# Kernel optimization log

Hardware: AMD Instinct MI355X
Metric: run time of the kernel (lower is better)

## Reference

```python
import jax, jax.numpy as jnp
import numpy as np

B, S, H = 2, 2048, 2048
NH, NKV, HD = 32, 8, 64
GROUPS = NH // NKV
SCALE = HD ** -0.5


def _rope_tables(key):
    # Real RoPE cos/sin tables (HF Llama style), shape [B, S, HD]
    inv_freq = 1.0 / (10000.0 ** (jnp.arange(0, HD, 2, dtype=jnp.float32) / HD))  # [HD/2]
    t = jnp.arange(S, dtype=jnp.float32)
    freqs = jnp.outer(t, inv_freq)                      # [S, HD/2]
    emb = jnp.concatenate([freqs, freqs], axis=-1)      # [S, HD]
    cos = jnp.broadcast_to(jnp.cos(emb)[None], (B, S, HD))
    sin = jnp.broadcast_to(jnp.sin(emb)[None], (B, S, HD))
    return cos, sin


def setup_inputs() -> dict:
    key = jax.random.key(0)
    ks = jax.random.split(key, 9)
    w = 0.02
    cos, sin = _rope_tables(key)
    return {
        "hidden_states": jax.random.normal(ks[0], (B, S, H), jnp.float32),
        "bounding_box_embeddings": jax.random.normal(ks[1], (B, S, H), jnp.float32),
        "cos": cos,
        "sin": sin,
        "Wq": jax.random.normal(ks[2], (H, NH * HD), jnp.float32) * w,
        "Wk": jax.random.normal(ks[3], (H, NKV * HD), jnp.float32) * w,
        "Wv": jax.random.normal(ks[4], (H, NKV * HD), jnp.float32) * w,
        "Wo": jax.random.normal(ks[5], (NH * HD, H), jnp.float32) * w,
        "Wsq": jax.random.normal(ks[6], (H, NH * HD), jnp.float32) * w,
        "Wsk": jax.random.normal(ks[7], (H, NKV * HD), jnp.float32) * w,
    }


def _rotate_half(x):
    x1, x2 = x[..., : HD // 2], x[..., HD // 2 :]
    return jnp.concatenate([-x2, x1], axis=-1)


def _apply_rope(q, k, cos, sin):
    # q: [B,NH,S,HD], k: [B,NKV,S,HD]; cos/sin [B,S,HD] -> broadcast over heads
    c = cos[:, None, :, :]
    s = sin[:, None, :, :]
    return q * c + _rotate_half(q) * s, k * c + _rotate_half(k) * s


def _proj_heads(x, W, n_heads):
    b, s, _ = x.shape
    return (x @ W).reshape(b, s, n_heads, HD).transpose(0, 2, 1, 3)  # [B,nh,S,HD]


def reference(hidden_states, bounding_box_embeddings, cos, sin, Wq, Wk, Wv, Wo, Wsq, Wsk):
    # Text Q/K/V with RoPE
    q = _proj_heads(hidden_states, Wq, NH)
    k = _proj_heads(hidden_states, Wk, NKV)
    v = _proj_heads(hidden_states, Wv, NKV)
    q, k = _apply_rope(q, k, cos, sin)
    # Spatial Q/K (no V) with RoPE
    sq = _proj_heads(bounding_box_embeddings, Wsq, NH)
    sk = _proj_heads(bounding_box_embeddings, Wsk, NKV)
    sq, sk = _apply_rope(sq, sk, cos, sin)
    # Fused text+spatial states, then GQA repeat_kv
    q = q + sq                                   # [B,NH,S,HD]
    k = jnp.repeat(k + sk, GROUPS, axis=1)       # [B,NH,S,HD]
    v = jnp.repeat(v, GROUPS, axis=1)            # [B,NH,S,HD]
    # Eager attention with causal mask
    scores = jnp.einsum("bhqd,bhkd->bhqk", q, k) * SCALE
    causal = jnp.tril(jnp.ones((S, S), dtype=bool))
    scores = jnp.where(causal[None, None], scores, jnp.finfo(jnp.float32).min)
    probs = jax.nn.softmax(scores.astype(jnp.float32), axis=-1).astype(q.dtype)
    attn = jnp.einsum("bhqk,bhkd->bhqd", probs, v)           # [B,NH,S,HD]
    attn = attn.transpose(0, 2, 1, 3).reshape(B, S, NH * HD)  # [B,S,NH*HD]
    return attn @ Wo
```

## Files before the change

### kernel.cpp

```cpp
#include <hip/hip_runtime.h>

#define B_ 2
#define S_ 2048
#define H_ 2048
#define NH_ 32
#define NKV_ 8
#define HD_ 64

typedef short short8 __attribute__((ext_vector_type(8)));
typedef float f32x4 __attribute__((ext_vector_type(4)));
typedef float f32x16 __attribute__((ext_vector_type(16)));
typedef unsigned int uint4v __attribute__((ext_vector_type(4)));

__device__ __forceinline__ float bf2f(unsigned short u) {
  union { unsigned int i; float f; } v; v.i = ((unsigned int)u) << 16; return v.f;
}
__device__ __forceinline__ unsigned short f2bf(float f) {
  union { float f; unsigned int i; } v; v.f = f;
  unsigned int u = v.i;
  u += 0x7fffu + ((u >> 16) & 1u);
  return (unsigned short)(u >> 16);
}
__device__ __forceinline__ unsigned int cvtpk(float lo, float hi) {
  unsigned int r;
  asm("v_cvt_pk_bf16_f32 %0, %1, %2" : "=v"(r) : "v"(lo), "v"(hi));
  return r;
}
__device__ __forceinline__ void pl32swap(unsigned int& a, unsigned int& b) {
  asm("v_permlane32_swap_b32 %0, %1" : "+v"(a), "+v"(b));
}
__device__ __forceinline__ short8 mkfrag(unsigned a, unsigned b, unsigned c, unsigned d) {
  union { uint4v u; short8 s; } x;
  x.u = (uint4v){a, b, c, d};
  return x.s;
}
__device__ __forceinline__ void gload_lds16(const unsigned short* g, unsigned short* l) {
  __builtin_amdgcn_global_load_lds((const __attribute__((address_space(1))) void*)g,
                                   (__attribute__((address_space(3))) void*)l,
                                   16, 0, 0);
}
#define MFMA32(A, B, C) __builtin_amdgcn_mfma_f32_32x32x16_bf16(A, B, C, 0, 0, 0)
#define BARF() asm volatile("s_barrier" ::: "memory")

__global__ __launch_bounds__(256) void castA_frag(const float* __restrict__ in,
                                                  unsigned short* __restrict__ out) {
  int c = blockIdx.x * 4 + (threadIdx.x >> 6);
  int l = threadIdx.x & 63;
  int D = c & 31, KT = (c >> 5) & 31, bm = c >> 10;
  int row = bm * 256 + ((D >> 4) & 1) * 128 + ((D >> 3) & 1) * 64 + ((D >> 1) & 3) * 16 + (l & 15);
  int k = KT * 64 + (D & 1) * 32 + (l >> 4) * 8;
  const float* src = in + (size_t)row * 2048 + k;
  float4 v0 = *(const float4*)src;
  float4 v1 = *(const float4*)(src + 4);
  ushort4 o0, o1;
  o0.x = f2bf(v0.x); o0.y = f2bf(v0.y); o0.z = f2bf(v0.z); o0.w = f2bf(v0.w);
  o1.x = f2bf(v1.x); o1.y = f2bf(v1.y); o1.z = f2bf(v1.z); o1.w = f2bf(v1.w);
  unsigned short* dst = out + (size_t)c * 512 + l * 8;
  *(ushort4*)dst = o0;
  *(ushort4*)(dst + 4) = o1;
}

__global__ __launch_bounds__(256) void castW_frag(const float* __restrict__ W0,
                                                  const float* __restrict__ W1,
                                                  const float* __restrict__ W2,
                                                  unsigned short* __restrict__ out) {
  __shared__ float tile[64][33];
  int c = blockIdx.x;
  int ngroup = c & 7, KT = (c >> 3) & 31, bn = c >> 8;
  int n0 = bn * 256 + ngroup * 32;
  const float* W; int Nw, nb;
  if (n0 < 2048)      { W = W0; Nw = 2048; nb = n0; }
  else if (n0 < 2560) { W = W1; Nw = 512;  nb = n0 - 2048; }
  else                { W = W2; Nw = 512;  nb = n0 - 2560; }
  int t = threadIdx.x;
  int col = t & 31, r8 = t >> 5;
#pragma unroll
  for (int p = 0; p < 8; ++p) {
    int kk = p * 8 + r8;
    tile[kk][col] = W[(size_t)(KT * 64 + kk) * Nw + nb + col];
  }
  __syncthreads();
  int e = t >> 6, l = t & 63;
  int nf = e >> 1, ks = e & 1;
  ushort4 o0, o1;
  unsigned short* op = (unsigned short*)&o0;
#pragma unroll
  for (int j = 0; j < 8; ++j) {
    unsigned short v = f2bf(tile[ks * 32 + (l >> 4) * 8 + j][nf * 16 + (l & 15)]);
    if (j < 4) op[j] = v; else ((unsigned short*)&o1)[j - 4] = v;
  }
  unsigned short* dst = out + (((size_t)(c >> 3) * 32 + ngroup * 4 + e) << 9) + l * 8;
  *(ushort4*)dst = o0;
  *(ushort4*)(dst + 4) = o1;
}

__global__ __launch_bounds__(256) void transpose_cast(const float* __restrict__ W,
                                                      unsigned short* __restrict__ Wt,
                                                      int N, int K) {
  __shared__ float tile[32][33];
  int n0 = blockIdx.x * 32, k0 = blockIdx.y * 32;
  int tx = threadIdx.x & 31;
  int ty = threadIdx.x >> 5;
#pragma unroll
  for (int i = 0; i < 32; i += 8)
    tile[ty + i][tx] = W[(size_t)(k0 + ty + i) * N + n0 + tx];
  __syncthreads();
#pragma unroll
  for (int i = 0; i < 32; i += 8)
    Wt[(size_t)(n0 + ty + i) * K + k0 + tx] = f2bf(tile[tx][ty + i]);
}

__global__ __launch_bounds__(256) void vtrans_kernel(const unsigned short* __restrict__ P1,
                                                     unsigned short* __restrict__ Vt) {
  __shared__ unsigned short tile[32][33];
  int s0 = blockIdx.x * 32, d0 = blockIdx.y * 32, bk = blockIdx.z;
  int b = bk >> 3, kv = bk & 7;
  int tx = threadIdx.x & 31, ty = threadIdx.x >> 5;
#pragma unroll
  for (int i = 0; i < 32; i += 8)
    tile[ty + i][tx] = P1[(size_t)(b * S_ + s0 + ty + i) * 3072 + 2560 + kv * 64 + d0 + tx];
  __syncthreads();
#pragma unroll
  for (int i = 0; i < 32; i += 8)
    Vt[(size_t)(bk * 64 + d0 + ty + i) * S_ + s0 + tx] = tile[tx][ty + i];
}

__global__ __launch_bounds__(256) void combine_rope(const unsigned short* __restrict__ P1,
                                                    const unsigned short* __restrict__ P2,
                                                    const float* __restrict__ cosT,
                                                    const float* __restrict__ sinT,
                                                    unsigned short* __restrict__ Qb,
                                                    unsigned short* __restrict__ Kb) {
  int id = blockIdx.x * 256 + threadIdx.x;
  int row = id / 640;
  int grp = id - row * 640;
  int b = row >> 11;
  int s = row & 2047;
  bool isQ = grp < 512;
  int n = isQ ? grp * 4 : (grp - 512) * 4;
  int h = n >> 6;
  int d = n & 63;
  int base = isQ ? 0 : 2048;
  const int ld1 = 3072, ld2 = 2560;
  int pd = (d < 32) ? d + 32 : d - 32;
  float sign = (d < 32) ? -1.f : 1.f;
  int pcol = base + h * 64 + pd;

  ushort4 a1 = *(const ushort4*)&P1[(size_t)row * ld1 + base + n];
  ushort4 a2 = *(const ushort4*)&P2[(size_t)row * ld2 + base + n];
  ushort4 b1 = *(const ushort4*)&P1[(size_t)row * ld1 + pcol];
  ushort4 b2 = *(const ushort4*)&P2[(size_t)row * ld2 + pcol];
  float4 cv = *(const float4*)&cosT[(size_t)row * 64 + d];
  float4 sv = *(const float4*)&sinT[(size_t)row * 64 + d];
  float scale = isQ ? 0.125f : 1.0f;

  float xs[4] = { bf2f(a1.x) + bf2f(a2.x), bf2f(a1.y) + bf2f(a2.y),
                  bf2f(a1.z) + bf2f(a2.z), bf2f(a1.w) + bf2f(a2.w) };
  float xp[4] = { bf2f(b1.x) + bf2f(b2.x), bf2f(b1.y) + bf2f(b2.y),
                  bf2f(b1.z) + bf2f(b2.z), bf2f(b1.w) + bf2f(b2.w) };
  float cc[4] = { cv.x, cv.y, cv.z, cv.w };
  float ss[4] = { sv.x, sv.y, sv.z, sv.w };
  ushort4 o;
  unsigned short* op = (unsigned short*)&o;
#pragma unroll
  for (int i = 0; i < 4; ++i)
    op[i] = f2bf((xs[i] * cc[i] + sign * xp[i] * ss[i]) * scale);

  if (isQ)
    *(ushort4*)&Qb[((size_t)(b * NH_ + h) * S_ + s) * HD_ + d] = o;
  else
    *(ushort4*)&Kb[((size_t)(b * NKV_ + h) * S_ + s) * HD_ + d] = o;
}


#define RD_A(BC, MH) do { \
  _Pragma("unroll") for (int mf = 0; mf < 4; ++mf) { \
    _Pragma("unroll") for (int ks = 0; ks < 2; ++ks) \
      a[mf][ks] = *(const short8*)&lds[BC][((wm * 2 + (MH)) * 8 + mf * 2 + ks) * 512 + l * 8]; \
  } \
} while (0)

#define RD_B(BC, NH, DST) do { \
  _Pragma("unroll") for (int nf = 0; nf < 2; ++nf) { \
    _Pragma("unroll") for (int ks = 0; ks < 2; ++ks) \
      DST[nf][ks] = *(const short8*)&lds[BC][16384 + (((wn * 2 + (NH)) * 2 + nf) * 2 + ks) * 512 + l * 8]; \
  } \
} while (0)

#define MM(MH, NH, BB) do { \
  _Pragma("unroll") for (int mf = 0; mf < 4; ++mf) { \
    _Pragma("unroll") for (int nf = 0; nf < 2; ++nf) { \
      _Pragma("unroll") for (int ks = 0; ks < 2; ++ks) \
        acc[(MH) * 4 + mf][(NH) * 2 + nf] = __builtin_amdgcn_mfma_f32_16x16x32_bf16( \
            a[mf][ks], BB[nf][ks], acc[(MH) * 4 + mf][(NH) * 2 + nf], 0, 0, 0); \
    } \
  } \
} while (0)

#define STAGE_A(H, KT) do { \
  int bq_ = (KT) & 1; \
  int d1_ = (H) * 8 + w; \
  gload_lds16(aF + (((size_t)((KT) * 32 + d1_)) << 9), &lds[bq_][d1_ * 512]); \
  gload_lds16(aF + (((size_t)((KT) * 32 + 16 + d1_)) << 9), &lds[bq_][(16 + d1_) * 512]); \
} while (0)

#define STAGE_B(H, KT) do { \
  int bq_ = (KT) & 1; \
  int e1_ = (w >> 2) * 8 + (H) * 4 + (w & 3); \
  gload_lds16(bF + (((size_t)((KT) * 32 + e1_)) << 9), &lds[bq_][16384 + e1_ * 512]); \
  gload_lds16(bF + (((size_t)((KT) * 32 + 16 + e1_)) << 9), &lds[bq_][16384 + (16 + e1_) * 512]); \
} while (0)

#define GROUP_P(BC, G) do { \
  int kt1 = (G) + 1; if (kt1 > 31) kt1 = 31; \
  int kt2 = (G) + 2; if (kt2 > 31) kt2 = 31; \
  int BN_ = kt1 & 1; \
   \
  BARF(); \
  __builtin_amdgcn_s_setprio(1); MM(0, 0, b0); __builtin_amdgcn_s_setprio(0); \
  RD_B(BC, 1, b1); \
  STAGE_A(1, kt1); \
   \
  BARF(); \
  __builtin_amdgcn_s_setprio(1); MM(0, 1, b1); __builtin_amdgcn_s_setprio(0); \
  STAGE_A(0, kt2); \
   \
  BARF(); \
  RD_A(BC, 1); \
  __builtin_amdgcn_s_setprio(1); MM(1, 0, b0); __builtin_amdgcn_s_setprio(0); \
  STAGE_B(0, kt2); \
  asm volatile("s_waitcnt vmcnt(8)" ::: "memory"); \
   \
  BARF(); \
  __builtin_amdgcn_s_setprio(1); MM(1, 1, b1); __builtin_amdgcn_s_setprio(0); \
  RD_A(BN_, 0); \
  RD_B(BN_, 0, b0); \
  STAGE_B(1, kt2); \
  asm volatile("s_waitcnt vmcnt(6)" ::: "memory"); \
} while (0)

template <int OF32>
__global__ __launch_bounds__(512, 2) void gemm256(const unsigned short* __restrict__ Afr,
                                                  const unsigned short* __restrict__ Wfr,
                                                  void* __restrict__ Cv,
                                                  int N, int nbx) {
  __shared__ unsigned short lds[2][32768];
  int nwg = gridDim.x;
  int orig = blockIdx.x;
  int wgid = (orig & 7) * (nwg >> 3) + (orig >> 3);
  int bn = wgid % nbx, bm = wgid / nbx;
  int t = threadIdx.x, w = t >> 6, l = t & 63;
  int wm = w >> 2, wn = w & 3;

  const unsigned short* aF = Afr + ((size_t)bm << 19) + l * 8;
  const unsigned short* bF = Wfr + ((size_t)bn << 19) + l * 8;

  short8 a[4][2], b0[2][2], b1[2][2];
  f32x4 acc[8][4];
#pragma unroll
  for (int mi = 0; mi < 8; ++mi)
#pragma unroll
    for (int ni = 0; ni < 4; ++ni) acc[mi][ni] = 0.f;

  STAGE_A(0, 0); STAGE_A(1, 0); STAGE_B(0, 0); STAGE_B(1, 0);
  STAGE_A(0, 1); STAGE_B(0, 1); STAGE_B(1, 1);
  asm volatile("s_waitcnt vmcnt(6)" ::: "memory");
  BARF();
  RD_A(0, 0);
  RD_B(0, 0, b0);

  for (int tg = 0; tg < 32; tg += 2) {
    GROUP_P(0, tg);
    GROUP_P(1, tg + 1);
  }
  asm volatile("s_waitcnt vmcnt(0)" ::: "memory");

#pragma unroll
  for (int mi = 0; mi < 8; ++mi) {
    int row = bm * 256 + wm * 128 + (mi >> 2) * 64 + (mi & 3) * 16 + (l >> 4) * 4;
#pragma unroll
    for (int ni = 0; ni < 4; ++ni) {
      int col = bn * 256 + wn * 64 + (ni >> 1) * 32 + (ni & 1) * 16 + (l & 15);
#pragma unroll
      for (int r = 0; r < 4; ++r) {
        if constexpr (OF32)
          ((float*)Cv)[(size_t)(row + r) * N + col] = acc[mi][ni][r];
        else
          ((unsigned short*)Cv)[(size_t)(row + r) * N + col] = f2bf(acc[mi][ni][r]);
      }
    }
  }
}

#define RD_BN(BC) do { \
  _Pragma("unroll") for (int nf = 0; nf < 2; ++nf) { \
    _Pragma("unroll") for (int ks = 0; ks < 2; ++ks) \
      bb[nf][ks] = *(const short8*)&lds2[BC][16384 + ((wn * 2 + nf) * 2 + ks) * 512 + l * 8]; \
  } \
} while (0)

#define RD_AN(BC, MH) do { \
  _Pragma("unroll") for (int mf = 0; mf < 4; ++mf) { \
    _Pragma("unroll") for (int ks = 0; ks < 2; ++ks) \
      a[mf][ks] = *(const short8*)&lds2[BC][((wm * 2 + (MH)) * 8 + mf * 2 + ks) * 512 + l * 8]; \
  } \
} while (0)

#define MMN(MH) do { \
  _Pragma("unroll") for (int mf = 0; mf < 4; ++mf) { \
    _Pragma("unroll") for (int nf = 0; nf < 2; ++nf) { \
      _Pragma("unroll") for (int ks = 0; ks < 2; ++ks) \
        acc[(MH) * 4 + mf][nf] = __builtin_amdgcn_mfma_f32_16x16x32_bf16( \
            a[mf][ks], bb[nf][ks], acc[(MH) * 4 + mf][nf], 0, 0, 0); \
    } \
  } \
} while (0)

#define STAGE_AU(Q, KT) do { \
  int bq_ = (KT) & 1; \
  gload_lds16((((Q) < 2) ? srcA0 : srcA1) + (size_t)((Q) & 1) * (64 * 2048) + (size_t)(KT) * 64, \
              &lds2[bq_][(((Q) >> 1) * 16 + ((Q) & 1) * 8 + w) * 512]); \
} while (0)

#define STAGE_BU(H, KT) do { \
  int bq_ = (KT) & 1; \
  gload_lds16(srcB0 + (size_t)(H) * (32 * 2048) + (size_t)(KT) * 64, \
              &lds2[bq_][16384 + ((w >> 2) * 8 + (H) * 4 + (w & 3)) * 512]); \
} while (0)

#define GROUPN(BC, G) do { \
  int kt1 = (G) + 1; if (kt1 > 31) kt1 = 31; \
  int kt2 = (G) + 2; if (kt2 > 31) kt2 = 31; \
  RD_AN(BC, 0); RD_BN(BC); \
  STAGE_AU(1, kt1); STAGE_AU(3, kt1); \
  BARF(); \
  __builtin_amdgcn_s_setprio(1); MMN(0); __builtin_amdgcn_s_setprio(0); \
  BARF(); \
  RD_AN(BC, 1); \
  STAGE_AU(0, kt2); STAGE_AU(2, kt2); STAGE_BU(0, kt2); STAGE_BU(1, kt2); \
  BARF(); \
  __builtin_amdgcn_s_setprio(1); MMN(1); __builtin_amdgcn_s_setprio(0); \
  asm volatile("s_waitcnt vmcnt(4)" ::: "memory"); \
  BARF(); \
} while (0)

__global__ __launch_bounds__(512, 2) void gemm256n(const unsigned short* __restrict__ A,
                                                   const unsigned short* __restrict__ Bt,
                                                   float* __restrict__ C,
                                                   int N, int nbx) {
  __shared__ unsigned short lds2[2][24576];
  int nwg = gridDim.x;
  int orig = blockIdx.x;
  int wgid = (orig & 7) * (nwg >> 3) + (orig >> 3);
  int bn = wgid % nbx, bm = wgid / nbx;
  int t = threadIdx.x, w = t >> 6, l = t & 63;
  int wm = w >> 2, wn = w & 3;

  int kcol = (w & 1) * 32 + ((t >> 4) & 3) * 8;
  int rA0 = bm * 256 + ((w >> 1) & 3) * 16 + (t & 15);
  const unsigned short* srcA0 = A + (size_t)rA0 * 2048 + kcol;
  const unsigned short* srcA1 = srcA0 + (size_t)128 * 2048;
  int nB0 = bn * 128 + (w >> 2) * 64 + ((w >> 1) & 1) * 16 + (t & 15);
  const unsigned short* srcB0 = Bt + (size_t)nB0 * 2048 + kcol;

  short8 a[4][2], bb[2][2];
  f32x4 acc[8][2];
#pragma unroll
  for (int mi = 0; mi < 8; ++mi)
#pragma unroll
    for (int ni = 0; ni < 2; ++ni) acc[mi][ni] = 0.f;

  STAGE_AU(0, 0); STAGE_AU(1, 0); STAGE_AU(2, 0); STAGE_AU(3, 0); STAGE_BU(0, 0); STAGE_BU(1, 0);
  STAGE_AU(0, 1); STAGE_AU(2, 1); STAGE_BU(0, 1); STAGE_BU(1, 1);
  asm volatile("s_waitcnt vmcnt(4)" ::: "memory");
  BARF();

  for (int tg = 0; tg < 32; tg += 2) {
    GROUPN(0, tg);
    GROUPN(1, tg + 1);
  }
  asm volatile("s_waitcnt vmcnt(0)" ::: "memory");

#pragma unroll
  for (int mi = 0; mi < 8; ++mi) {
    int row = bm * 256 + wm * 128 + (mi >> 2) * 64 + (mi & 3) * 16 + (l >> 4) * 4;
#pragma unroll
    for (int nf = 0; nf < 2; ++nf) {
      int col = bn * 128 + wn * 32 + nf * 16 + (l & 15);
#pragma unroll
      for (int r = 0; r < 4; ++r)
        C[(size_t)(row + r) * N + col] = acc[mi][nf][r];
    }
  }
}

__global__ __launch_bounds__(512) void attn_kernel(const unsigned short* __restrict__ Q,
                                                   const unsigned short* __restrict__ K,
                                                   const unsigned short* __restrict__ Vt,
                                                   unsigned short* __restrict__ attnOut) {
  __shared__ unsigned short lK[2][64 * 64];
  __shared__ unsigned short lV[2][64 * 64];

  int bx = blockIdx.x;
  int j = bx & 7;
  int bh = bx >> 3;
  int head = bh & 31;
  int b = bh >> 5;
  int kvh = head >> 2;
  const unsigned short* Kp = K + (size_t)(b * NKV_ + kvh) * S_ * HD_;
  const unsigned short* Vp = Vt + (size_t)(b * NKV_ + kvh) * HD_ * S_;

  int t = threadIdx.x;
  int w = t >> 6, l = t & 63;
  int q32 = l & 31, hf = l >> 5;
  int qb_eff = (w < 4) ? j : (15 - j);
  int qbase_w = qb_eff * 128 + (w & 3) * 32;
  const unsigned short* Qp = Q + ((size_t)(b * NH_ + head) * S_ + qbase_w) * HD_;

  short8 qf[4];
  {
    const unsigned short* qrow = Qp + (size_t)q32 * HD_ + hf * 8;
#pragma unroll
    for (int kc = 0; kc < 4; ++kc)
      qf[kc] = *(const short8*)(qrow + kc * 16);
  }

  int srow = t >> 3;
  int sslot = t & 7;
  unsigned lOff = srow * 128 + ((sslot ^ (srow & 7)) << 4);
  const char* gK0 = (const char*)(Kp + (size_t)srow * 64 + sslot * 8);
  const char* gV0 = (const char*)(Vp + (size_t)srow * 2048 + sslot * 8);

  {
    int4 rk = *(const int4*)(gK0);
    int4 rv = *(const int4*)(gV0);
    *(int4*)((char*)lK[0] + lOff) = rk;
    *(int4*)((char*)lV[0] + lOff) = rv;
  }
  __syncthreads();

  f32x16 oA = 0.f, oB = 0.f;
  float mrun = -1e30f, lrun = 0.f;

  int nt = 32 - 2 * j;
  int cur = 0;
  for (int tI = 0; tI < nt; ++tI) {
    int kv0 = tI * 64;
    bool pf = (tI + 1 < nt);
    int4 nk, nv;
    if (pf) {
      nk = *(const int4*)(gK0 + (size_t)(kv0 + 64) * 128);
      nv = *(const int4*)(gV0 + (size_t)(kv0 + 64) * 2);
    }

    if (kv0 <= qbase_w + 31) {
      const char* lKc = (const char*)lK[cur];
      const char* lVc = (const char*)lV[cur];
      int swz = q32 & 7;

      f32x16 sA = 0.f, sB = 0.f;
      __builtin_amdgcn_s_setprio(1);
#pragma unroll
      for (int kc = 0; kc < 4; ++kc) {
        int cs = (kc << 1) | hf;
        short8 ak0 = *(const short8*)(lKc + q32 * 128 + ((cs ^ swz) << 4));
        short8 ak1 = *(const short8*)(lKc + (32 + q32) * 128 + ((cs ^ swz) << 4));
        sA = MFMA32(ak0, qf[kc], sA);
        sB = MFMA32(ak1, qf[kc], sB);
      }
      __builtin_amdgcn_s_setprio(0);

      if (kv0 + 63 > qbase_w) {
        int qg = qbase_w + q32;
#pragma unroll
        for (int r = 0; r < 16; ++r) {
          int kvr = kv0 + (r & 3) + ((r >> 2) << 3) + (hf << 2);
          if (kvr > qg) sA[r] = -1e30f;
          if (kvr + 32 > qg) sB[r] = -1e30f;
        }
      }

      float pmax = sA[0];
#pragma unroll
      for (int r = 1; r < 16; ++r) pmax = fmaxf(pmax, sA[r]);
#pragma unroll
      for (int r = 0; r < 16; ++r) pmax = fmaxf(pmax, sB[r]);
      pmax = fmaxf(pmax, __shfl_xor(pmax, 32, 64));

      if (!__all(pmax <= mrun + 8.f)) {
        float mnew = fmaxf(mrun, pmax);
        float sf = __expf(mrun - mnew);
        lrun *= sf;
        mrun = mnew;
#pragma unroll
        for (int r = 0; r < 16; ++r) {
          int src = (r & 3) + ((r >> 2) << 3) + (hf << 2);
          float sfr = __shfl(sf, src, 64);
          oA[r] *= sfr;
          oB[r] *= sfr;
        }
      }

      float rs = 0.f;
#pragma unroll
      for (int r = 0; r < 16; ++r) { sA[r] = __expf(sA[r] - mrun); rs += sA[r]; }
#pragma unroll
      for (int r = 0; r < 16; ++r) { sB[r] = __expf(sB[r] - mrun); rs += sB[r]; }
      rs += __shfl_xor(rs, 32, 64);
      lrun += rs;

      short8 paf[4];
      {
        unsigned c0 = cvtpk(sA[0], sA[1]), c1 = cvtpk(sA[2], sA[3]);
        unsigned c2 = cvtpk(sA[4], sA[5]), c3 = cvtpk(sA[6], sA[7]);
        pl32swap(c0, c2); pl32swap(c1, c3);
        paf[0] = mkfrag(c0, c1, c2, c3);
      }
      {
        unsigned c0 = cvtpk(sA[8], sA[9]),  c1 = cvtpk(sA[10], sA[11]);
        unsigned c2 = cvtpk(sA[12], sA[13]), c3 = cvtpk(sA[14], sA[15]);
        pl32swap(c0, c2); pl32swap(c1, c3);
        paf[1] = mkfrag(c0, c1, c2, c3);
      }
      {
        unsigned c0 = cvtpk(sB[0], sB[1]), c1 = cvtpk(sB[2], sB[3]);
        unsigned c2 = cvtpk(sB[4], sB[5]), c3 = cvtpk(sB[6], sB[7]);
        pl32swap(c0, c2); pl32swap(c1, c3);
        paf[2] = mkfrag(c0, c1, c2, c3);
      }
      {
        unsigned c0 = cvtpk(sB[8], sB[9]),  c1 = cvtpk(sB[10], sB[11]);
        unsigned c2 = cvtpk(sB[12], sB[13]), c3 = cvtpk(sB[14], sB[15]);
        pl32swap(c0, c2); pl32swap(c1, c3);
        paf[3] = mkfrag(c0, c1, c2, c3);
      }

      __builtin_amdgcn_s_setprio(1);
#pragma unroll
      for (int ks = 0; ks < 4; ++ks) {
        int cs = (ks << 1) | hf;
        short8 v0 = *(const short8*)(lVc + q32 * 128 + ((cs ^ swz) << 4));
        short8 v1 = *(const short8*)(lVc + (32 + q32) * 128 + ((cs ^ swz) << 4));
        oA = MFMA32(paf[ks], v0, oA);
        oB = MFMA32(paf[ks], v1, oB);
      }
      __builtin_amdgcn_s_setprio(0);
    }

    if (pf) {
      *(int4*)((char*)lK[cur ^ 1] + lOff) = nk;
      *(int4*)((char*)lV[cur ^ 1] + lOff) = nv;
    }
    __syncthreads();
    cur ^= 1;
  }

  float linv = 1.f / lrun;
#pragma unroll
  for (int r = 0; r < 16; ++r) {
    int src = (r & 3) + ((r >> 2) << 3) + (hf << 2);
    float li = __shfl(linv, src, 64);
    unsigned short* op = attnOut + ((size_t)(b * S_ + qbase_w + src)) * (NH_ * HD_) + head * 64;
    op[q32] = f2bf(oA[r] * li);
    op[32 + q32] = f2bf(oB[r] * li);
  }
}

extern "C" void kernel_launch(void* const* d_in, const int* in_sizes, int n_in,
                              void* d_out, int out_size, void* d_ws, size_t ws_size,
                              hipStream_t stream) {
  const float* hidden = (const float*)d_in[0];
  const float* bbox   = (const float*)d_in[1];
  const float* cosT   = (const float*)d_in[2];
  const float* sinT   = (const float*)d_in[3];
  const float* Wq  = (const float*)d_in[4];
  const float* Wk  = (const float*)d_in[5];
  const float* Wv  = (const float*)d_in[6];
  const float* Wo  = (const float*)d_in[7];
  const float* Wsq = (const float*)d_in[8];
  const float* Wsk = (const float*)d_in[9];

  char* ws = (char*)d_ws;
  size_t off = 0;
  auto alloc = [&](size_t bytes) {
    void* p = ws + off;
    off += (bytes + 255) & ~(size_t)255;
    return p;
  };
  unsigned short* AfrH = (unsigned short*)alloc((size_t)4096 * 2048 * 2);
  unsigned short* AfrB = (unsigned short*)alloc((size_t)4096 * 2048 * 2);
  unsigned short* WhF  = (unsigned short*)alloc((size_t)3072 * 2048 * 2);
  unsigned short* WbF  = (unsigned short*)alloc((size_t)2560 * 2048 * 2);
  unsigned short* WoT  = (unsigned short*)alloc((size_t)2048 * 2048 * 2);
  unsigned short* P1   = (unsigned short*)alloc((size_t)4096 * 3072 * 2);
  unsigned short* P2   = (unsigned short*)alloc((size_t)4096 * 2560 * 2);
  unsigned short* Qb   = AfrB;
  unsigned short* Kb   = AfrH;
  unsigned short* Vt   = AfrH + (size_t)B_ * NKV_ * S_ * HD_;
  unsigned short* attn = WhF;

  dim3 blk(256);
  castA_frag<<<dim3(4096), blk, 0, stream>>>(hidden, AfrH);
  castA_frag<<<dim3(4096), blk, 0, stream>>>(bbox,   AfrB);
  castW_frag<<<dim3(3072), blk, 0, stream>>>(Wq,  Wk,  Wv,      WhF);
  castW_frag<<<dim3(2560), blk, 0, stream>>>(Wsq, Wsk, nullptr, WbF);
  transpose_cast<<<dim3(64, 64), blk, 0, stream>>>(Wo, WoT, 2048, 2048);

  gemm256<0><<<dim3(192), dim3(512), 0, stream>>>(AfrH, WhF, P1, 3072, 12);
  gemm256<0><<<dim3(160), dim3(512), 0, stream>>>(AfrB, WbF, P2, 2560, 10);

  combine_rope<<<dim3((B_ * S_ * 640) / 256), blk, 0, stream>>>(P1, P2, cosT, sinT, Qb, Kb);
  vtrans_kernel<<<dim3(64, 2, 16), blk, 0, stream>>>(P1, Vt);

  attn_kernel<<<dim3(512), dim3(512), 0, stream>>>(Qb, Kb, Vt, attn);

  gemm256n<<<dim3(256), dim3(512), 0, stream>>>(attn, WoT, (float*)d_out, 2048, 16);
}
```

Baseline: 261.9 us.

## Write attention output in MFMA fragment layout and retile output projection GEMM

The attention kernel now stores its output directly in the pre-swizzled fragment layout that the output-projection GEMM loads with 16-byte global-to-LDS copies. Wo is converted with the shared fragment-cast kernel instead of a separate transpose kernel. The output GEMM changes from 256x128 to 128x256 tiles with a new staging schedule. Softmax also moves to exp2 with log2(e) folded into the Q scale and uses three-input max instructions. The scattered 2-byte stores from attention may cost more than the contiguous row stores they replace.

```diff
diff --git a/kernel.cpp b/kernel.cpp
--- a/kernel.cpp
+++ b/kernel.cpp
@@ -28,6 +28,11 @@
 }
 __device__ __forceinline__ void pl32swap(unsigned int& a, unsigned int& b) {
   asm("v_permlane32_swap_b32 %0, %1" : "+v"(a), "+v"(b));
+}
+__device__ __forceinline__ float fmax3(float a, float b, float c) {
+  float r;
+  asm("v_max3_f32 %0, %1, %2, %3" : "=v"(r) : "v"(a), "v"(b), "v"(c));
+  return r;
 }
 __device__ __forceinline__ short8 mkfrag(unsigned a, unsigned b, unsigned c, unsigned d) {
   union { uint4v u; short8 s; } x;
@@ -92,22 +97,6 @@
   unsigned short* dst = out + (((size_t)(c >> 3) * 32 + ngroup * 4 + e) << 9) + l * 8;
   *(ushort4*)dst = o0;
   *(ushort4*)(dst + 4) = o1;
-}
-
-__global__ __launch_bounds__(256) void transpose_cast(const float* __restrict__ W,
-                                                      unsigned short* __restrict__ Wt,
-                                                      int N, int K) {
-  __shared__ float tile[32][33];
-  int n0 = blockIdx.x * 32, k0 = blockIdx.y * 32;
-  int tx = threadIdx.x & 31;
-  int ty = threadIdx.x >> 5;
-#pragma unroll
-  for (int i = 0; i < 32; i += 8)
-    tile[ty + i][tx] = W[(size_t)(k0 + ty + i) * N + n0 + tx];
-  __syncthreads();
-#pragma unroll
-  for (int i = 0; i < 32; i += 8)
-    Wt[(size_t)(n0 + ty + i) * K + k0 + tx] = f2bf(tile[tx][ty + i]);
 }
 
 __global__ __launch_bounds__(256) void vtrans_kernel(const unsigned short* __restrict__ P1,
@@ -152,7 +141,7 @@
   ushort4 b2 = *(const ushort4*)&P2[(size_t)row * ld2 + pcol];
   float4 cv = *(const float4*)&cosT[(size_t)row * 64 + d];
   float4 sv = *(const float4*)&sinT[(size_t)row * 64 + d];
-  float scale = isQ ? 0.125f : 1.0f;
+  float scale = isQ ? 0.18033688f : 1.0f;
 
   float xs[4] = { bf2f(a1.x) + bf2f(a2.x), bf2f(a1.y) + bf2f(a2.y),
                   bf2f(a1.z) + bf2f(a2.z), bf2f(a1.w) + bf2f(a2.w) };
@@ -172,7 +161,6 @@
     *(ushort4*)&Kb[((size_t)(b * NKV_ + h) * S_ + s) * HD_ + d] = o;
 }
 
-
 #define RD_A(BC, MH) do { \
   _Pragma("unroll") for (int mf = 0; mf < 4; ++mf) { \
     _Pragma("unroll") for (int ks = 0; ks < 2; ++ks) \
@@ -215,22 +203,18 @@
   int kt1 = (G) + 1; if (kt1 > 31) kt1 = 31; \
   int kt2 = (G) + 2; if (kt2 > 31) kt2 = 31; \
   int BN_ = kt1 & 1; \
-   \
   BARF(); \
   __builtin_amdgcn_s_setprio(1); MM(0, 0, b0); __builtin_amdgcn_s_setprio(0); \
   RD_B(BC, 1, b1); \
   STAGE_A(1, kt1); \
-   \
   BARF(); \
   __builtin_amdgcn_s_setprio(1); MM(0, 1, b1); __builtin_amdgcn_s_setprio(0); \
   STAGE_A(0, kt2); \
-   \
   BARF(); \
   RD_A(BC, 1); \
   __builtin_amdgcn_s_setprio(1); MM(1, 0, b0); __builtin_amdgcn_s_setprio(0); \
   STAGE_B(0, kt2); \
   asm volatile("s_waitcnt vmcnt(8)" ::: "memory"); \
-   \
   BARF(); \
   __builtin_amdgcn_s_setprio(1); MM(1, 1, b1); __builtin_amdgcn_s_setprio(0); \
   RD_A(BN_, 0); \
@@ -239,7 +223,6 @@
   asm volatile("s_waitcnt vmcnt(6)" ::: "memory"); \
 } while (0)
 
-template <int OF32>
 __global__ __launch_bounds__(512, 2) void gemm256(const unsigned short* __restrict__ Afr,
                                                   const unsigned short* __restrict__ Wfr,
                                                   void* __restrict__ Cv,
@@ -282,73 +265,70 @@
     for (int ni = 0; ni < 4; ++ni) {
       int col = bn * 256 + wn * 64 + (ni >> 1) * 32 + (ni & 1) * 16 + (l & 15);
 #pragma unroll
-      for (int r = 0; r < 4; ++r) {
-        if constexpr (OF32)
-          ((float*)Cv)[(size_t)(row + r) * N + col] = acc[mi][ni][r];
-        else
-          ((unsigned short*)Cv)[(size_t)(row + r) * N + col] = f2bf(acc[mi][ni][r]);
-      }
+      for (int r = 0; r < 4; ++r)
+        ((unsigned short*)Cv)[(size_t)(row + r) * N + col] = f2bf(acc[mi][ni][r]);
     }
   }
 }
 
-#define RD_BN(BC) do { \
+#define RD_AO(BC) do { \
+  _Pragma("unroll") for (int mf = 0; mf < 4; ++mf) { \
+    _Pragma("unroll") for (int ks = 0; ks < 2; ++ks) \
+      a[mf][ks] = *(const short8*)&lds3[BC][(wm * 8 + mf * 2 + ks) * 512 + l * 8]; \
+  } \
+} while (0)
+
+#define RD_BO(BC, NH, DST) do { \
   _Pragma("unroll") for (int nf = 0; nf < 2; ++nf) { \
     _Pragma("unroll") for (int ks = 0; ks < 2; ++ks) \
-      bb[nf][ks] = *(const short8*)&lds2[BC][16384 + ((wn * 2 + nf) * 2 + ks) * 512 + l * 8]; \
+      DST[nf][ks] = *(const short8*)&lds3[BC][8192 + (((wn * 2 + (NH)) * 2 + nf) * 2 + ks) * 512 + l * 8]; \
   } \
 } while (0)
 
-#define RD_AN(BC, MH) do { \
-  _Pragma("unroll") for (int mf = 0; mf < 4; ++mf) { \
-    _Pragma("unroll") for (int ks = 0; ks < 2; ++ks) \
-      a[mf][ks] = *(const short8*)&lds2[BC][((wm * 2 + (MH)) * 8 + mf * 2 + ks) * 512 + l * 8]; \
-  } \
-} while (0)
-
-#define MMN(MH) do { \
+#define MM_O(NH, BB) do { \
   _Pragma("unroll") for (int mf = 0; mf < 4; ++mf) { \
     _Pragma("unroll") for (int nf = 0; nf < 2; ++nf) { \
       _Pragma("unroll") for (int ks = 0; ks < 2; ++ks) \
-        acc[(MH) * 4 + mf][nf] = __builtin_amdgcn_mfma_f32_16x16x32_bf16( \
-            a[mf][ks], bb[nf][ks], acc[(MH) * 4 + mf][nf], 0, 0, 0); \
+        acc[mf][(NH) * 2 + nf] = __builtin_amdgcn_mfma_f32_16x16x32_bf16( \
+            a[mf][ks], BB[nf][ks], acc[mf][(NH) * 2 + nf], 0, 0, 0); \
     } \
   } \
 } while (0)
 
-#define STAGE_AU(Q, KT) do { \
+#define STAGE_AO(KT) do { \
   int bq_ = (KT) & 1; \
-  gload_lds16((((Q) < 2) ? srcA0 : srcA1) + (size_t)((Q) & 1) * (64 * 2048) + (size_t)(KT) * 64, \
-              &lds2[bq_][(((Q) >> 1) * 16 + ((Q) & 1) * 8 + w) * 512]); \
-} while (0)
-
-#define STAGE_BU(H, KT) do { \
+  gload_lds16(aF + (((size_t)((KT) * 16 + w)) << 9), &lds3[bq_][w * 512]); \
+  gload_lds16(aF + (((size_t)((KT) * 16 + 8 + w)) << 9), &lds3[bq_][(8 + w) * 512]); \
+} while (0)
+
+#define STAGE_BO(H, KT) do { \
   int bq_ = (KT) & 1; \
-  gload_lds16(srcB0 + (size_t)(H) * (32 * 2048) + (size_t)(KT) * 64, \
-              &lds2[bq_][16384 + ((w >> 2) * 8 + (H) * 4 + (w & 3)) * 512]); \
-} while (0)
-
-#define GROUPN(BC, G) do { \
+  int e1_ = (w >> 2) * 8 + (H) * 4 + (w & 3); \
+  gload_lds16(bF + (((size_t)((KT) * 32 + e1_)) << 9), &lds3[bq_][8192 + e1_ * 512]); \
+  gload_lds16(bF + (((size_t)((KT) * 32 + 16 + e1_)) << 9), &lds3[bq_][8192 + (16 + e1_) * 512]); \
+} while (0)
+
+#define GROUPO(BC, G) do { \
   int kt1 = (G) + 1; if (kt1 > 31) kt1 = 31; \
   int kt2 = (G) + 2; if (kt2 > 31) kt2 = 31; \
-  RD_AN(BC, 0); RD_BN(BC); \
-  STAGE_AU(1, kt1); STAGE_AU(3, kt1); \
-  BARF(); \
-  __builtin_amdgcn_s_setprio(1); MMN(0); __builtin_amdgcn_s_setprio(0); \
-  BARF(); \
-  RD_AN(BC, 1); \
-  STAGE_AU(0, kt2); STAGE_AU(2, kt2); STAGE_BU(0, kt2); STAGE_BU(1, kt2); \
-  BARF(); \
-  __builtin_amdgcn_s_setprio(1); MMN(1); __builtin_amdgcn_s_setprio(0); \
+  RD_AO(BC); RD_BO(BC, 0, b0); \
+  STAGE_BO(1, kt1); \
+  BARF(); \
+  __builtin_amdgcn_s_setprio(1); MM_O(0, b0); __builtin_amdgcn_s_setprio(0); \
+  BARF(); \
+  RD_BO(BC, 1, b1); \
+  STAGE_AO(kt2); STAGE_BO(0, kt2); \
+  BARF(); \
+  __builtin_amdgcn_s_setprio(1); MM_O(1, b1); __builtin_amdgcn_s_setprio(0); \
   asm volatile("s_waitcnt vmcnt(4)" ::: "memory"); \
   BARF(); \
 } while (0)
 
-__global__ __launch_bounds__(512, 2) void gemm256n(const unsigned short* __restrict__ A,
-                                                   const unsigned short* __restrict__ Bt,
-                                                   float* __restrict__ C,
-                                                   int N, int nbx) {
-  __shared__ unsigned short lds2[2][24576];
+__global__ __launch_bounds__(512, 2) void gemm_op(const unsigned short* __restrict__ Afr,
+                                                  const unsigned short* __restrict__ Wfr,
+                                                  float* __restrict__ C,
+                                                  int N, int nbx) {
+  __shared__ unsigned short lds3[2][24576];
   int nwg = gridDim.x;
   int orig = blockIdx.x;
   int wgid = (orig & 7) * (nwg >> 3) + (orig >> 3);
@@ -356,40 +336,36 @@
   int t = threadIdx.x, w = t >> 6, l = t & 63;
   int wm = w >> 2, wn = w & 3;
 
-  int kcol = (w & 1) * 32 + ((t >> 4) & 3) * 8;
-  int rA0 = bm * 256 + ((w >> 1) & 3) * 16 + (t & 15);
-  const unsigned short* srcA0 = A + (size_t)rA0 * 2048 + kcol;
-  const unsigned short* srcA1 = srcA0 + (size_t)128 * 2048;
-  int nB0 = bn * 128 + (w >> 2) * 64 + ((w >> 1) & 1) * 16 + (t & 15);
-  const unsigned short* srcB0 = Bt + (size_t)nB0 * 2048 + kcol;
-
-  short8 a[4][2], bb[2][2];
-  f32x4 acc[8][2];
-#pragma unroll
-  for (int mi = 0; mi < 8; ++mi)
-#pragma unroll
-    for (int ni = 0; ni < 2; ++ni) acc[mi][ni] = 0.f;
-
-  STAGE_AU(0, 0); STAGE_AU(1, 0); STAGE_AU(2, 0); STAGE_AU(3, 0); STAGE_BU(0, 0); STAGE_BU(1, 0);
-  STAGE_AU(0, 1); STAGE_AU(2, 1); STAGE_BU(0, 1); STAGE_BU(1, 1);
+  const unsigned short* aF = Afr + ((size_t)bm << 18) + l * 8;
+  const unsigned short* bF = Wfr + ((size_t)bn << 19) + l * 8;
+
+  short8 a[4][2], b0[2][2], b1[2][2];
+  f32x4 acc[4][4];
+#pragma unroll
+  for (int mi = 0; mi < 4; ++mi)
+#pragma unroll
+    for (int ni = 0; ni < 4; ++ni) acc[mi][ni] = 0.f;
+
+  STAGE_AO(0); STAGE_BO(0, 0); STAGE_BO(1, 0);
+  STAGE_AO(1); STAGE_BO(0, 1);
   asm volatile("s_waitcnt vmcnt(4)" ::: "memory");
   BARF();
 
   for (int tg = 0; tg < 32; tg += 2) {
-    GROUPN(0, tg);
-    GROUPN(1, tg + 1);
+    GROUPO(0, tg);
+    GROUPO(1, tg + 1);
   }
   asm volatile("s_waitcnt vmcnt(0)" ::: "memory");
 
 #pragma unroll
-  for (int mi = 0; mi < 8; ++mi) {
-    int row = bm * 256 + wm * 128 + (mi >> 2) * 64 + (mi & 3) * 16 + (l >> 4) * 4;
-#pragma unroll
-    for (int nf = 0; nf < 2; ++nf) {
-      int col = bn * 128 + wn * 32 + nf * 16 + (l & 15);
+  for (int mf = 0; mf < 4; ++mf) {
+    int row = bm * 128 + wm * 64 + mf * 16 + (l >> 4) * 4;
+#pragma unroll
+    for (int ni = 0; ni < 4; ++ni) {
+      int col = bn * 256 + wn * 64 + (ni >> 1) * 32 + (ni & 1) * 16 + (l & 15);
 #pragma unroll
       for (int r = 0; r < 4; ++r)
-        C[(size_t)(row + r) * N + col] = acc[mi][nf][r];
+        C[(size_t)(row + r) * N + col] = acc[mf][ni][r];
     }
   }
 }
@@ -397,7 +373,7 @@
 __global__ __launch_bounds__(512) void attn_kernel(const unsigned short* __restrict__ Q,
                                                    const unsigned short* __restrict__ K,
                                                    const unsigned short* __restrict__ Vt,
-                                                   unsigned short* __restrict__ attnOut) {
+                                                   unsigned short* __restrict__ attnF) {
   __shared__ unsigned short lK[2][64 * 64];
   __shared__ unsigned short lV[2][64 * 64];
 
@@ -480,16 +456,17 @@
         }
       }
 
-      float pmax = sA[0];
-#pragma unroll
-      for (int r = 1; r < 16; ++r) pmax = fmaxf(pmax, sA[r]);
-#pragma unroll
-      for (int r = 0; r < 16; ++r) pmax = fmaxf(pmax, sB[r]);
+      float pmax = fmax3(sA[0], sA[1], sA[2]);
+#pragma unroll
+      for (int r = 3; r < 15; r += 2) pmax = fmax3(pmax, sA[r], sA[r + 1]);
+      pmax = fmaxf(pmax, sA[15]);
+#pragma unroll
+      for (int r = 0; r < 16; r += 2) pmax = fmax3(pmax, sB[r], sB[r + 1]);
       pmax = fmaxf(pmax, __shfl_xor(pmax, 32, 64));
 
       if (!__all(pmax <= mrun + 8.f)) {
         float mnew = fmaxf(mrun, pmax);
-        float sf = __expf(mrun - mnew);
+        float sf = exp2f(mrun - mnew);
         lrun *= sf;
         mrun = mnew;
 #pragma unroll
@@ -503,9 +480,9 @@
 
       float rs = 0.f;
 #pragma unroll
-      for (int r = 0; r < 16; ++r) { sA[r] = __expf(sA[r] - mrun); rs += sA[r]; }
-#pragma unroll
-      for (int r = 0; r < 16; ++r) { sB[r] = __expf(sB[r] - mrun); rs += sB[r]; }
+      for (int r = 0; r < 16; ++r) { sA[r] = exp2f(sA[r] - mrun); rs += sA[r]; }
+#pragma unroll
+      for (int r = 0; r < 16; ++r) { sB[r] = exp2f(sB[r] - mrun); rs += sB[r]; }
       rs += __shfl_xor(rs, 32, 64);
       lrun += rs;
 
@@ -560,9 +537,13 @@
   for (int r = 0; r < 16; ++r) {
     int src = (r & 3) + ((r >> 2) << 3) + (hf << 2);
     float li = __shfl(linv, src, 64);
-    unsigned short* op = attnOut + ((size_t)(b * S_ + qbase_w + src)) * (NH_ * HD_) + head * 64;
-    op[q32] = f2bf(oA[r] * li);
-    op[32 + q32] = f2bf(oB[r] * li);
+    int R = b * S_ + qbase_w + src;
+    int bm = R >> 7;
+    int Dbase = (((R >> 6) & 1) << 3) | (((R >> 4) & 3) << 1);
+    int lp = ((q32 >> 3) << 4) | (R & 15);
+    size_t addr = (((size_t)(bm * 32 + head) * 16 + Dbase) << 9) + lp * 8 + (q32 & 7);
+    attnF[addr] = f2bf(oA[r] * li);
+    attnF[addr + 512] = f2bf(oB[r] * li);
   }
 }
 
@@ -591,28 +572,28 @@
   unsigned short* AfrB = (unsigned short*)alloc((size_t)4096 * 2048 * 2);
   unsigned short* WhF  = (unsigned short*)alloc((size_t)3072 * 2048 * 2);
   unsigned short* WbF  = (unsigned short*)alloc((size_t)2560 * 2048 * 2);
-  unsigned short* WoT  = (unsigned short*)alloc((size_t)2048 * 2048 * 2);
+  unsigned short* WoF  = (unsigned short*)alloc((size_t)2048 * 2048 * 2);
   unsigned short* P1   = (unsigned short*)alloc((size_t)4096 * 3072 * 2);
   unsigned short* P2   = (unsigned short*)alloc((size_t)4096 * 2560 * 2);
-  unsigned short* Qb   = AfrB;
-  unsigned short* Kb   = AfrH;
-  unsigned short* Vt   = AfrH + (size_t)B_ * NKV_ * S_ * HD_;
-  unsigned short* attn = WhF;
+  unsigned short* Qb    = AfrB;
+  unsigned short* Kb    = AfrH;
+  unsigned short* Vt    = AfrH + (size_t)B_ * NKV_ * S_ * HD_;
+  unsigned short* attnF = WhF;
 
   dim3 blk(256);
   castA_frag<<<dim3(4096), blk, 0, stream>>>(hidden, AfrH);
   castA_frag<<<dim3(4096), blk, 0, stream>>>(bbox,   AfrB);
   castW_frag<<<dim3(3072), blk, 0, stream>>>(Wq,  Wk,  Wv,      WhF);
   castW_frag<<<dim3(2560), blk, 0, stream>>>(Wsq, Wsk, nullptr, WbF);
-  transpose_cast<<<dim3(64, 64), blk, 0, stream>>>(Wo, WoT, 2048, 2048);
-
-  gemm256<0><<<dim3(192), dim3(512), 0, stream>>>(AfrH, WhF, P1, 3072, 12);
-  gemm256<0><<<dim3(160), dim3(512), 0, stream>>>(AfrB, WbF, P2, 2560, 10);
+  castW_frag<<<dim3(2048), blk, 0, stream>>>(Wo,  Wo,  Wo,      WoF);
+
+  gemm256<<<dim3(192), dim3(512), 0, stream>>>(AfrH, WhF, P1, 3072, 12);
+  gemm256<<<dim3(160), dim3(512), 0, stream>>>(AfrB, WbF, P2, 2560, 10);
 
   combine_rope<<<dim3((B_ * S_ * 640) / 256), blk, 0, stream>>>(P1, P2, cosT, sinT, Qb, Kb);
   vtrans_kernel<<<dim3(64, 2, 16), blk, 0, stream>>>(P1, Vt);
 
-  attn_kernel<<<dim3(512), dim3(512), 0, stream>>>(Qb, Kb, Vt, attn);
-
-  gemm256n<<<dim3(256), dim3(512), 0, stream>>>(attn, WoT, (float*)d_out, 2048, 16);
-}
+  attn_kernel<<<dim3(512), dim3(512), 0, stream>>>(Qb, Kb, Vt, attnF);
+
+  gemm_op<<<dim3(256), dim3(512), 0, stream>>>(attnF, WoF, (float*)d_out, 2048, 8);
+}
```

Result: slower. 296.5 us (+13.2%).
